# Performance work log

Measured on AMD Instinct MI355X. Metric: run time of the kernel, lower is better.

## Reference

```python
import jax, jax.numpy as jnp
import numpy as np

B = 131072      # batch size
H = 300         # hidden_dim (per-source), se has 2*H = 600 columns
T = 2           # num_source_tasks
EPS = 1e-20


def setup_inputs() -> dict:
    key = jax.random.key(0)
    k1, k2, k3, k4, k5 = jax.random.split(key, 5)
    return {
        "se1": jax.random.normal(k1, (B, H), dtype=jnp.float32),
        "se2": jax.random.normal(k2, (B, H), dtype=jnp.float32),
        "W": jax.random.normal(k3, (T, 2 * H), dtype=jnp.float32) / np.sqrt(2 * H).astype(np.float32),
        "b": jax.random.normal(k4, (T,), dtype=jnp.float32),
        "u": jax.random.uniform(k5, (B, T), dtype=jnp.float32),
        "n_tasks": 2,
    }


def reference(se1, se2, W, b, u, n_tasks):
    # se = torch.cat(se, dim=1) -> [B, 2H]
    se = jnp.concatenate([se1, se2], axis=1)
    # tiny linear + relu + log_softmax
    se_postrelu = jax.nn.relu(se @ W.T + b)            # [B, T]
    logits = jax.nn.log_softmax(se_postrelu, axis=1)   # [B, T]
    # straight-through gumbel-softmax (temperature=1.0, no mask)
    gumbel = -jnp.log(-jnp.log(u + EPS) + EPS)
    y = jax.nn.softmax(logits + gumbel, axis=1)        # soft probs
    y_hard = jax.nn.one_hot(jnp.argmax(y, axis=1), T, dtype=y.dtype)
    selector = jax.lax.stop_gradient(y_hard - y) + y   # ST estimator, [B, T]
    # rf: first H cols = selector[:,0], next H cols = selector[:,1]
    rf = jnp.repeat(selector, H, axis=1)               # [B, 2H]
    return se * rf
```

## Files before the change

### kernel.cpp

```cpp
#include <hip/hip_runtime.h>
#include <math.h>

typedef float f4 __attribute__((ext_vector_type(4)));

#define BDIM 256
#define WPB 4
#define RPW 4
#define ROWS_PER_BLOCK (WPB * RPW)
#define WAVE_F4 300

typedef __attribute__((address_space(1))) const unsigned int glob_u32;
typedef __attribute__((address_space(3))) unsigned int lds_u32;

__device__ __forceinline__ void gload16(const f4* g, f4* l) {
    __builtin_amdgcn_global_load_lds((glob_u32*)g, (lds_u32*)l, 16, 0, 0);
}

__device__ __forceinline__ float dot4(f4 a, f4 w) {
    return a[0]*w[0] + a[1]*w[1] + a[2]*w[2] + a[3]*w[3];
}

__global__ __launch_bounds__(BDIM) void taskselector_kernel(
    const f4* __restrict__ se1,
    const f4* __restrict__ se2,
    const float* __restrict__ W,
    const float* __restrict__ bvec,
    const f4* __restrict__ u4,
    f4* __restrict__ out)
{
    __shared__ f4 L1[WPB][WAVE_F4];
    __shared__ f4 L2[WPB][WAVE_F4];

    const int tid  = threadIdx.x;
    const int lane = tid & 63;
    const int wave = tid >> 6;
    const int rowbase = blockIdx.x * ROWS_PER_BLOCK + wave * RPW;

    f4* Lw1 = &L1[wave][0];
    f4* Lw2 = &L2[wave][0];

    const f4* g1 = se1 + (size_t)rowbase * 75;
    const f4* g2 = se2 + (size_t)rowbase * 75;
    #pragma unroll
    for (int k = 0; k < 4; k++) gload16(g1 + k * 64 + lane, Lw1 + k * 64);
    if (lane < 44)              gload16(g1 + 256 + lane,    Lw1 + 256);
    #pragma unroll
    for (int k = 0; k < 4; k++) gload16(g2 + k * 64 + lane, Lw2 + k * 64);
    if (lane < 44)              gload16(g2 + 256 + lane,    Lw2 + 256);

    const bool extra = (lane < 11);
    const f4 zero = (f4)0.f;
    const f4* W0 = (const f4*)W;
    const f4* W1 = (const f4*)(W + 600);
    f4 w0a = W0[lane];
    f4 w0b = extra ? W0[64 + lane]  : zero;
    f4 w0c = W0[75 + lane];
    f4 w0d = extra ? W0[139 + lane] : zero;
    f4 w1a = W1[lane];
    f4 w1b = extra ? W1[64 + lane]  : zero;
    f4 w1c = W1[75 + lane];
    f4 w1d = extra ? W1[139 + lane] : zero;
    const float b0 = bvec[0];
    const float b1 = bvec[1];
    const f4 ua = u4[rowbase / 2];
    const f4 ub = u4[rowbase / 2 + 1];

    asm volatile("s_waitcnt vmcnt(0)" ::: "memory");

    float s0r[1], dummy; (void)dummy; (void)s0r;
    float sA0, sA1, sB0, sB1, sC0, sC1, sD0, sD1;
    #pragma unroll
    for (int r = 0; r < RPW; r++) {
        f4 a0 = Lw1[r * 75 + lane];
        f4 c0 = Lw2[r * 75 + lane];
        f4 a1 = extra ? Lw1[r * 75 + 64 + lane] : zero;
        f4 c1 = extra ? Lw2[r * 75 + 64 + lane] : zero;
        float d0 = dot4(a0, w0a) + dot4(a1, w0b) + dot4(c0, w0c) + dot4(c1, w0d);
        float d1 = dot4(a0, w1a) + dot4(a1, w1b) + dot4(c0, w1c) + dot4(c1, w1d);
        #pragma unroll
        for (int off = 32; off > 0; off >>= 1) {
            d0 += __shfl_xor(d0, off, 64);
            d1 += __shfl_xor(d1, off, 64);
        }
        float z0 = fmaxf(d0 + b0, 0.f);
        float z1 = fmaxf(d1 + b1, 0.f);
        float m  = fmaxf(z0, z1);
        float lse = m + logf(expf(z0 - m) + expf(z1 - m));
        float uu0 = (r < 2) ? ((r == 0) ? ua[0] : ua[2]) : ((r == 2) ? ub[0] : ub[2]);
        float uu1 = (r < 2) ? ((r == 0) ? ua[1] : ua[3]) : ((r == 2) ? ub[1] : ub[3]);
        float q0 = (z0 - lse) + (-logf(-logf(uu0 + 1e-20f) + 1e-20f));
        float q1 = (z1 - lse) + (-logf(-logf(uu1 + 1e-20f) + 1e-20f));
        float mm = fmaxf(q0, q1);
        float e0 = expf(q0 - mm);
        float e1 = expf(q1 - mm);
        float s  = e0 + e1;
        float y0 = e0 / s;
        float y1 = e1 / s;
        bool  pick0 = (q0 >= q1);
        float s0 = pick0 ? ((1.f - y0) + y0) : 0.f;
        float s1 = pick0 ? 0.f : ((1.f - y1) + y1);
        if (r == 0) { sA0 = s0; sA1 = s1; }
        else if (r == 1) { sB0 = s0; sB1 = s1; }
        else if (r == 2) { sC0 = s0; sC1 = s1; }
        else { sD0 = s0; sD1 = s1; }
    }

    f4* o = out + (size_t)rowbase * 150;
    #pragma unroll
    for (int k = 0; k < 10; k++) {
        const int j = k * 64 + lane;
        if (k == 9 && lane >= 24) break;
        const int row = j / 150;
        const int rem = j - row * 150;
        const bool first = (rem < 75);
        f4 v = first ? Lw1[row * 75 + rem] : Lw2[row * 75 + rem - 75];
        float sf = (row < 2) ? ((row == 0) ? sA0 : sB0) : ((row == 2) ? sC0 : sD0);
        float ss = (row < 2) ? ((row == 0) ? sA1 : sB1) : ((row == 2) ? sC1 : sD1);
        float sc = first ? sf : ss;
        __builtin_nontemporal_store(v * sc, o + j);
    }
}

extern "C" void kernel_launch(void* const* d_in, const int* in_sizes, int n_in,
                              void* d_out, int out_size, void* d_ws, size_t ws_size,
                              hipStream_t stream) {
    const f4* se1 = (const f4*)d_in[0];
    const f4* se2 = (const f4*)d_in[1];
    const float* W = (const float*)d_in[2];
    const float* b = (const float*)d_in[3];
    const f4* u4  = (const f4*)d_in[4];
    f4* out = (f4*)d_out;

    const int Brows = in_sizes[0] / 300;
    const int nblocks = Brows / ROWS_PER_BLOCK;

    taskselector_kernel<<<nblocks, BDIM, 0, stream>>>(se1, se2, W, b, u4, out);
}
```

Measured before the change: 128.0 us.

## Replace LDS staging with per-wave register loads of row pairs and shuffle-based output

Each wave now handles two rows and loads them straight into registers with nontemporal global loads, replacing the global-to-LDS async copy path and the LDS buffers. Output rows are assembled by cross-lane shuffles that realign the 75-f4 row segments to the contiguous output layout. The aim is to drop LDS traffic and the full vmcnt wait, and to raise occupancy by using smaller blocks of work with no shared memory. In exchange, each wave keeps fewer bytes in flight and the kernel adds many shuffle instructions.

```diff
diff --git a/kernel.cpp b/kernel.cpp
--- a/kernel.cpp
+++ b/kernel.cpp
@@ -4,23 +4,21 @@
 typedef float f4 __attribute__((ext_vector_type(4)));
 
 #define BDIM 256
-#define WPB 4
-#define RPW 4
-#define ROWS_PER_BLOCK (WPB * RPW)
-#define WAVE_F4 300
-
-typedef __attribute__((address_space(1))) const unsigned int glob_u32;
-typedef __attribute__((address_space(3))) unsigned int lds_u32;
-
-__device__ __forceinline__ void gload16(const f4* g, f4* l) {
-    __builtin_amdgcn_global_load_lds((glob_u32*)g, (lds_u32*)l, 16, 0, 0);
-}
 
 __device__ __forceinline__ float dot4(f4 a, f4 w) {
     return a[0]*w[0] + a[1]*w[1] + a[2]*w[2] + a[3]*w[3];
 }
 
-__global__ __launch_bounds__(BDIM) void taskselector_kernel(
+__device__ __forceinline__ f4 rot4(f4 v, int src) {
+    f4 r;
+    r[0] = __shfl(v[0], src, 64);
+    r[1] = __shfl(v[1], src, 64);
+    r[2] = __shfl(v[2], src, 64);
+    r[3] = __shfl(v[3], src, 64);
+    return r;
+}
+
+__global__ __launch_bounds__(BDIM, 4) void taskselector_kernel(
     const f4* __restrict__ se1,
     const f4* __restrict__ se2,
     const float* __restrict__ W,
@@ -28,68 +26,63 @@
     const f4* __restrict__ u4,
     f4* __restrict__ out)
 {
-    __shared__ f4 L1[WPB][WAVE_F4];
-    __shared__ f4 L2[WPB][WAVE_F4];
-
     const int tid  = threadIdx.x;
     const int lane = tid & 63;
     const int wave = tid >> 6;
-    const int rowbase = blockIdx.x * ROWS_PER_BLOCK + wave * RPW;
+    const int k    = blockIdx.x * 4 + wave;
 
-    f4* Lw1 = &L1[wave][0];
-    f4* Lw2 = &L2[wave][0];
+    const f4 zero = (f4)0.f;
+    const bool lt11 = (lane < 11);
+    const bool lt22 = (lane < 22);
 
-    const f4* g1 = se1 + (size_t)rowbase * 75;
-    const f4* g2 = se2 + (size_t)rowbase * 75;
-    #pragma unroll
-    for (int k = 0; k < 4; k++) gload16(g1 + k * 64 + lane, Lw1 + k * 64);
-    if (lane < 44)              gload16(g1 + 256 + lane,    Lw1 + 256);
-    #pragma unroll
-    for (int k = 0; k < 4; k++) gload16(g2 + k * 64 + lane, Lw2 + k * 64);
-    if (lane < 44)              gload16(g2 + 256 + lane,    Lw2 + 256);
+    const f4* C1 = se1 + (size_t)k * 150;
+    const f4* C2 = se2 + (size_t)k * 150;
+    f4 v0 = __builtin_nontemporal_load(C1 + lane);
+    f4 v1 = __builtin_nontemporal_load(C1 + 64 + lane);
+    f4 v2 = lt22 ? __builtin_nontemporal_load(C1 + 128 + lane) : zero;
+    f4 v3 = __builtin_nontemporal_load(C2 + lane);
+    f4 v4 = __builtin_nontemporal_load(C2 + 64 + lane);
+    f4 v5 = lt22 ? __builtin_nontemporal_load(C2 + 128 + lane) : zero;
+    f4 uu = u4[k];
 
-    const bool extra = (lane < 11);
-    const f4 zero = (f4)0.f;
-    const f4* W0 = (const f4*)W;
-    const f4* W1 = (const f4*)(W + 600);
-    f4 w0a = W0[lane];
-    f4 w0b = extra ? W0[64 + lane]  : zero;
-    f4 w0c = W0[75 + lane];
-    f4 w0d = extra ? W0[139 + lane] : zero;
-    f4 w1a = W1[lane];
-    f4 w1b = extra ? W1[64 + lane]  : zero;
-    f4 w1c = W1[75 + lane];
-    f4 w1d = extra ? W1[139 + lane] : zero;
+    const f4* Wf0 = (const f4*)W;
+    const f4* Wf1 = (const f4*)(W + 600);
+    const int iB1 = lt11 ? 64 + lane : lane - 11;
+    const int iB2 = lt11 ? 139 + lane : 64 + lane;
+    f4 wA1_0 = Wf0[lane],      wA1_1 = Wf1[lane];
+    f4 wA2_0 = Wf0[75 + lane], wA2_1 = Wf1[75 + lane];
+    f4 wB1_0 = Wf0[iB1],       wB1_1 = Wf1[iB1];
+    f4 wB2_0 = Wf0[iB2],       wB2_1 = Wf1[iB2];
+    f4 wC1_0 = lt22 ? Wf0[53 + lane]  : zero;
+    f4 wC1_1 = lt22 ? Wf1[53 + lane]  : zero;
+    f4 wC2_0 = lt22 ? Wf0[128 + lane] : zero;
+    f4 wC2_1 = lt22 ? Wf1[128 + lane] : zero;
     const float b0 = bvec[0];
     const float b1 = bvec[1];
-    const f4 ua = u4[rowbase / 2];
-    const f4 ub = u4[rowbase / 2 + 1];
 
-    asm volatile("s_waitcnt vmcnt(0)" ::: "memory");
+    float dB0 = dot4(v1, wB1_0) + dot4(v4, wB2_0);
+    float dB1 = dot4(v1, wB1_1) + dot4(v4, wB2_1);
+    float p00 = dot4(v0, wA1_0) + dot4(v3, wA2_0) + (lt11 ? dB0 : 0.f);
+    float p01 = dot4(v0, wA1_1) + dot4(v3, wA2_1) + (lt11 ? dB1 : 0.f);
+    float p10 = (lt11 ? 0.f : dB0) + dot4(v2, wC1_0) + dot4(v5, wC2_0);
+    float p11 = (lt11 ? 0.f : dB1) + dot4(v2, wC1_1) + dot4(v5, wC2_1);
 
-    float s0r[1], dummy; (void)dummy; (void)s0r;
-    float sA0, sA1, sB0, sB1, sC0, sC1, sD0, sD1;
     #pragma unroll
-    for (int r = 0; r < RPW; r++) {
-        f4 a0 = Lw1[r * 75 + lane];
-        f4 c0 = Lw2[r * 75 + lane];
-        f4 a1 = extra ? Lw1[r * 75 + 64 + lane] : zero;
-        f4 c1 = extra ? Lw2[r * 75 + 64 + lane] : zero;
-        float d0 = dot4(a0, w0a) + dot4(a1, w0b) + dot4(c0, w0c) + dot4(c1, w0d);
-        float d1 = dot4(a0, w1a) + dot4(a1, w1b) + dot4(c0, w1c) + dot4(c1, w1d);
-        #pragma unroll
-        for (int off = 32; off > 0; off >>= 1) {
-            d0 += __shfl_xor(d0, off, 64);
-            d1 += __shfl_xor(d1, off, 64);
-        }
-        float z0 = fmaxf(d0 + b0, 0.f);
-        float z1 = fmaxf(d1 + b1, 0.f);
+    for (int off = 32; off > 0; off >>= 1) {
+        p00 += __shfl_xor(p00, off, 64);
+        p01 += __shfl_xor(p01, off, 64);
+        p10 += __shfl_xor(p10, off, 64);
+        p11 += __shfl_xor(p11, off, 64);
+    }
+
+    float sel00, sel01, sel10, sel11;
+    {
+        float z0 = fmaxf(p00 + b0, 0.f);
+        float z1 = fmaxf(p01 + b1, 0.f);
         float m  = fmaxf(z0, z1);
         float lse = m + logf(expf(z0 - m) + expf(z1 - m));
-        float uu0 = (r < 2) ? ((r == 0) ? ua[0] : ua[2]) : ((r == 2) ? ub[0] : ub[2]);
-        float uu1 = (r < 2) ? ((r == 0) ? ua[1] : ua[3]) : ((r == 2) ? ub[1] : ub[3]);
-        float q0 = (z0 - lse) + (-logf(-logf(uu0 + 1e-20f) + 1e-20f));
-        float q1 = (z1 - lse) + (-logf(-logf(uu1 + 1e-20f) + 1e-20f));
+        float q0 = (z0 - lse) + (-logf(-logf(uu[0] + 1e-20f) + 1e-20f));
+        float q1 = (z1 - lse) + (-logf(-logf(uu[1] + 1e-20f) + 1e-20f));
         float mm = fmaxf(q0, q1);
         float e0 = expf(q0 - mm);
         float e1 = expf(q1 - mm);
@@ -97,28 +90,45 @@
         float y0 = e0 / s;
         float y1 = e1 / s;
         bool  pick0 = (q0 >= q1);
-        float s0 = pick0 ? ((1.f - y0) + y0) : 0.f;
-        float s1 = pick0 ? 0.f : ((1.f - y1) + y1);
-        if (r == 0) { sA0 = s0; sA1 = s1; }
-        else if (r == 1) { sB0 = s0; sB1 = s1; }
-        else if (r == 2) { sC0 = s0; sC1 = s1; }
-        else { sD0 = s0; sD1 = s1; }
+        sel00 = pick0 ? ((1.f - y0) + y0) : 0.f;
+        sel01 = pick0 ? 0.f : ((1.f - y1) + y1);
+    }
+    {
+        float z0 = fmaxf(p10 + b0, 0.f);
+        float z1 = fmaxf(p11 + b1, 0.f);
+        float m  = fmaxf(z0, z1);
+        float lse = m + logf(expf(z0 - m) + expf(z1 - m));
+        float q0 = (z0 - lse) + (-logf(-logf(uu[2] + 1e-20f) + 1e-20f));
+        float q1 = (z1 - lse) + (-logf(-logf(uu[3] + 1e-20f) + 1e-20f));
+        float mm = fmaxf(q0, q1);
+        float e0 = expf(q0 - mm);
+        float e1 = expf(q1 - mm);
+        float s  = e0 + e1;
+        float y0 = e0 / s;
+        float y1 = e1 / s;
+        bool  pick0 = (q0 >= q1);
+        sel10 = pick0 ? ((1.f - y0) + y0) : 0.f;
+        sel11 = pick0 ? 0.f : ((1.f - y1) + y1);
     }
 
-    f4* o = out + (size_t)rowbase * 150;
-    #pragma unroll
-    for (int k = 0; k < 10; k++) {
-        const int j = k * 64 + lane;
-        if (k == 9 && lane >= 24) break;
-        const int row = j / 150;
-        const int rem = j - row * 150;
-        const bool first = (rem < 75);
-        f4 v = first ? Lw1[row * 75 + rem] : Lw2[row * 75 + rem - 75];
-        float sf = (row < 2) ? ((row == 0) ? sA0 : sB0) : ((row == 2) ? sC0 : sD0);
-        float ss = (row < 2) ? ((row == 0) ? sA1 : sB1) : ((row == 2) ? sC1 : sD1);
-        float sc = first ? sf : ss;
-        __builtin_nontemporal_store(v * sc, o + j);
-    }
+    const int r11 = (lane + 53) & 63;
+    const int r22 = (lane + 42) & 63;
+    f4 v1r = rot4(v1, r11);
+    f4 v2r = rot4(v2, r11);
+    f4 v3r = rot4(v3, r11);
+    f4 v4r = rot4(v4, r11);
+    f4 v4s = rot4(v4, r22);
+    f4 v5s = rot4(v5, r22);
+
+    f4* O = out + (size_t)k * 300;
+    __builtin_nontemporal_store(v0 * sel00, O + lane);
+    __builtin_nontemporal_store(lt11 ? v1 * sel00 : v3r * sel01, O + 64 + lane);
+    __builtin_nontemporal_store(
+        lt11 ? v3r * sel01 : (lt22 ? v4r * sel01 : v1r * sel10), O + 128 + lane);
+    __builtin_nontemporal_store(
+        lt11 ? v1r * sel10 : ((lane < 33) ? v2r * sel10 : v4s * sel11), O + 192 + lane);
+    if (lane < 44)
+        __builtin_nontemporal_store(lt22 ? v4s * sel11 : v5s * sel11, O + 256 + lane);
 }
 
 extern "C" void kernel_launch(void* const* d_in, const int* in_sizes, int n_in,
@@ -131,8 +141,9 @@
     const f4* u4  = (const f4*)d_in[4];
     f4* out = (f4*)d_out;
 
-    const int Brows = in_sizes[0] / 300;
-    const int nblocks = Brows / ROWS_PER_BLOCK;
+    const int Brows  = in_sizes[0] / 300;
+    const int pairs  = Brows / 2;
+    const int blocks = pairs / 4;
 
-    taskselector_kernel<<<nblocks, BDIM, 0, stream>>>(se1, se2, W, b, u4, out);
+    taskselector_kernel<<<blocks, BDIM, 0, stream>>>(se1, se2, W, b, u4, out);
 }
```

Measured after the change: 125.7 us. Within noise of the previous version (-1.8%).
